# Kernel tuning notes

Measured on AMD Instinct MI355X. Metric: run time of the kernel, lower is better.

## Reference

```python
import jax, jax.numpy as jnp
import numpy as np

N, H, FIN, FOUT = 4096, 8, 128, 64
NEG = -1e9


def setup_inputs() -> dict:
    key = jax.random.key(0)
    ks = jax.random.split(key, 6)
    x = jax.random.normal(ks[0], (N, FIN), dtype=jnp.float32)
    # dense additive adjacency mask: 0 where edge exists, -1e9 otherwise; self-loops on diagonal
    edge = jax.random.uniform(ks[1], (N, N)) < 0.02
    edge = edge | jnp.eye(N, dtype=bool)
    topology = jnp.where(edge, 0.0, NEG).astype(jnp.float32)
    # xavier-ish scaled params
    proj = jax.random.normal(ks[2], (H, FIN, FOUT), dtype=jnp.float32) * (2.0 / (FIN + FOUT)) ** 0.5
    a_src = jax.random.normal(ks[3], (H, FOUT, 1), dtype=jnp.float32) * (2.0 / (FOUT + 1)) ** 0.5
    a_tgt = jax.random.normal(ks[4], (H, FOUT, 1), dtype=jnp.float32) * (2.0 / (FOUT + 1)) ** 0.5
    skip_w = jax.random.normal(ks[5], (H * FOUT, FIN), dtype=jnp.float32) * (1.0 / FIN) ** 0.5
    return {"x": x, "topology": topology, "proj": proj, "a_src": a_src,
            "a_tgt": a_tgt, "skip_w": skip_w}


def reference(x, topology, proj, a_src, a_tgt, skip_w):
    lrelu = lambda v: jax.nn.leaky_relu(v, negative_slope=0.2)
    # projected node features per head: [H, N, FOUT]  (dropout is identity in eval)
    p = jnp.einsum('nf,hfo->hno', x, proj)
    # additive attention scores
    s_src = jnp.einsum('hno,hoi->hn', p, a_src)  # [H, N]
    s_tgt = jnp.einsum('hno,hoi->hn', p, a_tgt)  # [H, N]
    e = lrelu(s_src[:, :, None] + s_tgt[:, None, :])  # [H, N, N]
    attn = jax.nn.softmax(e + topology[None], axis=-1)  # masked row softmax
    # weighted aggregation -> [N, H, FOUT]
    out = jnp.einsum('hnm,hmo->nho', attn, p)
    # skip connection: Fin != Fout so project input
    out = out + (x @ skip_w.T).reshape(N, H, FOUT)
    # heads are averaged (to_aggregate_heads=False), then LeakyReLU
    out = lrelu(jnp.mean(out, axis=1))  # [N, FOUT]
    return out
```

## Files before the change

### kernel.cpp

```cpp
#include <hip/hip_runtime.h>
#include <hip/hip_bf16.h>
#include <cstdint>

#define N_NODES 4096
#define FIN     128
#define FOUT    64
#define NHEAD   8
#define C_TOT   512
#define ECAP    192
#define LDK     136

typedef float fx4    __attribute__((ext_vector_type(4)));
typedef short bf16x8 __attribute__((ext_vector_type(8)));
typedef float f32x4  __attribute__((ext_vector_type(4)));

__device__ __forceinline__ float lrelu(float v){ return v > 0.f ? v : 0.2f*v; }

__device__ __forceinline__ ushort f2b(float f){
    uint u = __float_as_uint(f);
    return (ushort)((u + 0x7FFFu + ((u >> 16) & 1u)) >> 16);
}

__global__ __launch_bounds__(256) void k_gemm(const float* __restrict__ x,
        const float* __restrict__ proj, const float* __restrict__ skip_w,
        const float* __restrict__ a_src, const float* __restrict__ a_tgt,
        __hip_bfloat16* __restrict__ pb, float* __restrict__ s_src_t,
        float* __restrict__ s_tgt_t, float* __restrict__ skipbar){
    __shared__ ushort xs[64*LDK];
    __shared__ ushort bs[64*LDK];
    int tid = threadIdx.x;
    int n0  = blockIdx.x * 64;
    int h   = blockIdx.y;

    #pragma unroll
    for (int k=0; k<8; k++){
        int q = tid + k*256;
        int r = q >> 5, f0 = (q & 31)*4;
        float4 v = *(const float4*)(x + (size_t)(n0+r)*FIN + f0);
        ushort4 u = make_ushort4(f2b(v.x), f2b(v.y), f2b(v.z), f2b(v.w));
        *(ushort4*)(xs + r*LDK + f0) = u;
    }
    if (h < 8){
        const float* B = proj + (size_t)h*FIN*FOUT;
        #pragma unroll
        for (int k=0; k<8; k++){
            int q = tid + k*256;
            int f = q >> 4, o0 = (q & 15)*4;
            float4 v = *(const float4*)(B + f*64 + o0);
            bs[(o0+0)*LDK + f] = f2b(v.x);
            bs[(o0+1)*LDK + f] = f2b(v.y);
            bs[(o0+2)*LDK + f] = f2b(v.z);
            bs[(o0+3)*LDK + f] = f2b(v.w);
        }
    } else {
        #pragma unroll
        for (int k=0; k<8; k++){
            int q = tid + k*256;
            int o = q >> 5, f0 = (q & 31)*4;
            float sx=0.f, sy=0.f, sz=0.f, sw=0.f;
            #pragma unroll
            for (int hh=0; hh<8; hh++){
                float4 v = *(const float4*)(skip_w + (size_t)(hh*64+o)*FIN + f0);
                sx += v.x; sy += v.y; sz += v.z; sw += v.w;
            }
            ushort4 u = make_ushort4(f2b(sx*0.125f), f2b(sy*0.125f),
                                     f2b(sz*0.125f), f2b(sw*0.125f));
            *(ushort4*)(bs + o*LDK + f0) = u;
        }
    }
    __syncthreads();

    int lane = tid & 63, w = tid >> 6;
    int r16 = lane & 15, kg = lane >> 4;
    f32x4 acc[4] = {{0.f,0.f,0.f,0.f},{0.f,0.f,0.f,0.f},
                    {0.f,0.f,0.f,0.f},{0.f,0.f,0.f,0.f}};
    const ushort* arow = xs + (w*16 + r16)*LDK + kg*8;
    #pragma unroll
    for (int ks=0; ks<4; ks++){
        bf16x8 a = *(const bf16x8*)(arow + ks*32);
        #pragma unroll
        for (int ct=0; ct<4; ct++){
            bf16x8 b = *(const bf16x8*)(bs + (ct*16 + r16)*LDK + ks*32 + kg*8);
            acc[ct] = __builtin_amdgcn_mfma_f32_16x16x32_bf16(a, b, acc[ct], 0, 0, 0);
        }
    }

    int rowbase = n0 + w*16 + kg*4;
    if (h < 8){
        float as[4], at[4];
        #pragma unroll
        for (int ct=0; ct<4; ct++){
            as[ct] = a_src[h*64 + ct*16 + r16];
            at[ct] = a_tgt[h*64 + ct*16 + r16];
        }
        ushort* pbu = (ushort*)pb;
        #pragma unroll
        for (int r=0; r<4; r++){
            float vs = 0.f, vt = 0.f;
            #pragma unroll
            for (int ct=0; ct<4; ct++){
                float v = acc[ct][r];
                vs = fmaf(v, as[ct], vs);
                vt = fmaf(v, at[ct], vt);
                pbu[(size_t)(rowbase+r)*C_TOT + (ct*16 + r16)*8 + h] = f2b(v);
            }
            #pragma unroll
            for (int off=1; off<16; off<<=1){
                vs += __shfl_xor(vs, off);
                vt += __shfl_xor(vt, off);
            }
            if (r16 == 0){
                s_src_t[(size_t)(rowbase+r)*8 + h] = vs;
                s_tgt_t[(size_t)(rowbase+r)*8 + h] = vt;
            }
        }
    } else {
        #pragma unroll
        for (int r=0; r<4; r++)
            #pragma unroll
            for (int ct=0; ct<4; ct++)
                skipbar[(size_t)(rowbase+r)*FOUT + ct*16 + r16] = acc[ct][r];
    }
}

__global__ __launch_bounds__(256) void k_fused(const float* __restrict__ topo,
        const __hip_bfloat16* __restrict__ pb, const float* __restrict__ s_src_t,
        const float* __restrict__ s_tgt_t, const float* __restrict__ skipbar,
        float* __restrict__ out){
    __shared__ float  wlds[4*ECAP*8];
    __shared__ ushort jlds[4*ECAP];

    int lane = threadIdx.x & 63, w = threadIdx.x >> 6;
    int i    = blockIdx.x*4 + w;
    float*  wp = wlds + w*(ECAP*8);
    ushort* jp = jlds + w*ECAP;

    jp[lane] = 0; jp[64+lane] = 0; jp[128+lane] = 0;

    const fx4* tp = (const fx4*)(topo + (size_t)i*N_NODES);
    unsigned long long m = 0;
    #pragma unroll
    for (int k=0; k<16; k++){
        fx4 v = __builtin_nontemporal_load(&tp[k*64 + lane]);
        unsigned b = 0;
        b |= (v.x==0.f) ? 1u : 0u;
        b |= (v.y==0.f) ? 2u : 0u;
        b |= (v.z==0.f) ? 4u : 0u;
        b |= (v.w==0.f) ? 8u : 0u;
        m |= ((unsigned long long)b) << (k*4);
    }

    int cnt = __popcll(m);
    int pre = cnt;
    #pragma unroll
    for (int off=1; off<64; off<<=1){
        int t = __shfl_up(pre, off);
        if (lane >= off) pre += t;
    }
    int ne = __shfl(pre, 63);
    if (ne > ECAP) ne = ECAP;
    {
        int base = pre - cnt;
        unsigned long long mm = m;
        while (mm){
            int b = __builtin_ctzll(mm);
            mm &= mm - 1;
            if (base < ECAP)
                jp[base] = (ushort)((b>>2)*256 + lane*4 + (b&3));
            base++;
        }
    }

    float4 ss0 = *(const float4*)(s_src_t + (size_t)i*8);
    float4 ss1 = *(const float4*)(s_src_t + (size_t)i*8 + 4);
    float ssrc[8] = {ss0.x,ss0.y,ss0.z,ss0.w,ss1.x,ss1.y,ss1.z,ss1.w};

    float st[3][8];
    #pragma unroll
    for (int s=0; s<3; s++){
        int e = s*64 + lane;
        bool act = e < ne;
        int j = act ? (int)jp[e] : 0;
        const float4* tpp = (const float4*)(s_tgt_t + (size_t)j*8);
        float4 a = tpp[0], b = tpp[1];
        st[s][0] = act ? a.x : -3.0e38f;
        st[s][1] = act ? a.y : -3.0e38f;
        st[s][2] = act ? a.z : -3.0e38f;
        st[s][3] = act ? a.w : -3.0e38f;
        st[s][4] = act ? b.x : -3.0e38f;
        st[s][5] = act ? b.y : -3.0e38f;
        st[s][6] = act ? b.z : -3.0e38f;
        st[s][7] = act ? b.w : -3.0e38f;
    }
    float M[8];
    #pragma unroll
    for (int hh=0; hh<8; hh++)
        M[hh] = fmaxf(fmaxf(st[0][hh], st[1][hh]), st[2][hh]);
    #pragma unroll
    for (int off=32; off; off>>=1)
        #pragma unroll
        for (int hh=0; hh<8; hh++)
            M[hh] = fmaxf(M[hh], __shfl_xor(M[hh], off));
    #pragma unroll
    for (int hh=0; hh<8; hh++)
        M[hh] = lrelu(ssrc[hh] + M[hh]);

    float den[8] = {0.f,0.f,0.f,0.f,0.f,0.f,0.f,0.f};
    #pragma unroll
    for (int s=0; s<3; s++){
        int e = s*64 + lane;
        bool act = e < ne;
        float wv[8];
        #pragma unroll
        for (int hh=0; hh<8; hh++){
            float z = ssrc[hh] + st[s][hh];
            z = z > 0.f ? z : 0.2f*z;
            float ww = __expf(z - M[hh]);
            ww = act ? ww : 0.f;
            den[hh] += ww;
            wv[hh] = ww;
        }
        *(float4*)(wp + e*8)     = make_float4(wv[0],wv[1],wv[2],wv[3]);
        *(float4*)(wp + e*8 + 4) = make_float4(wv[4],wv[5],wv[6],wv[7]);
    }
    #pragma unroll
    for (int off=32; off; off>>=1)
        #pragma unroll
        for (int hh=0; hh<8; hh++)
            den[hh] += __shfl_xor(den[hh], off);

    float acc[8] = {0.f,0.f,0.f,0.f,0.f,0.f,0.f,0.f};
    const char* pbb = (const char*)pb;
    uint laneoff = (uint)lane * 16;
    int ne8 = (ne + 7) & ~7;
    for (int e0=0; e0<ne8; e0+=8){
        int jj[8];
        #pragma unroll
        for (int k=0; k<8; k++) jj[k] = (int)jp[e0+k];
        uint4 d[8];
        #pragma unroll
        for (int k=0; k<8; k++)
            d[k] = *(const uint4*)(pbb + ((size_t)(uint)jj[k] << 10) + laneoff);
        #pragma unroll
        for (int k=0; k<8; k++){
            float4 wa = *(const float4*)(wp + (e0+k)*8);
            float4 wb = *(const float4*)(wp + (e0+k)*8 + 4);
            acc[0] = fmaf(wa.x, __uint_as_float(d[k].x << 16), acc[0]);
            acc[1] = fmaf(wa.y, __uint_as_float(d[k].x),       acc[1]);
            acc[2] = fmaf(wa.z, __uint_as_float(d[k].y << 16), acc[2]);
            acc[3] = fmaf(wa.w, __uint_as_float(d[k].y),       acc[3]);
            acc[4] = fmaf(wb.x, __uint_as_float(d[k].z << 16), acc[4]);
            acc[5] = fmaf(wb.y, __uint_as_float(d[k].z),       acc[5]);
            acc[6] = fmaf(wb.z, __uint_as_float(d[k].w << 16), acc[6]);
            acc[7] = fmaf(wb.w, __uint_as_float(d[k].w),       acc[7]);
        }
    }

    float s = 0.f;
    #pragma unroll
    for (int hh=0; hh<8; hh++) s += acc[hh] / den[hh];
    float o = s*0.125f + skipbar[(size_t)i*64 + lane];
    out[(size_t)i*64 + lane] = lrelu(o);
}

extern "C" void kernel_launch(void* const* d_in, const int* in_sizes, int n_in,
                              void* d_out, int out_size, void* d_ws, size_t ws_size,
                              hipStream_t stream){
    const float* x      = (const float*)d_in[0];
    const float* topo   = (const float*)d_in[1];
    const float* proj   = (const float*)d_in[2];
    const float* a_src  = (const float*)d_in[3];
    const float* a_tgt  = (const float*)d_in[4];
    const float* skip_w = (const float*)d_in[5];
    float* out = (float*)d_out;

    char* ws = (char*)d_ws;
    __hip_bfloat16* pb = (__hip_bfloat16*)ws;
    float*  skipbar = (float*)(ws + (4u<<20));
    float*  s_src_t = (float*)(ws + (5u<<20));
    float*  s_tgt_t = (float*)(ws + (5u<<20) + (128u<<10));

    hipLaunchKernelGGL(k_gemm,  dim3(64, 9), dim3(256), 0, stream, x, proj, skip_w,
                       a_src, a_tgt, pb, s_src_t, s_tgt_t, skipbar);
    hipLaunchKernelGGL(k_fused, dim3(1024),  dim3(256), 0, stream, topo, pb,
                       s_src_t, s_tgt_t, skipbar, out);
}
```

Before: 47.99 us.

## Split fused kernel into producer wave scanning topology and consumer waves aggregating

Each block now handles 8 nodes. One wave streams the topology rows and builds the neighbour index lists in shared memory, signalling readiness with workgroup-scope release/acquire flags. The other three waves compute the softmax and the aggregation, overlapping the mask scan with the gather/FMA work. Attention weights are stored in shared memory as bf16 to cut LDS footprint, and the index lists are read as vectors. The risk is that a single producer wave per block limits how much of the dominant topology stream is in flight, adds spin-wait overhead, and slightly lowers weight precision.

```diff
diff --git a/kernel.cpp b/kernel.cpp
--- a/kernel.cpp
+++ b/kernel.cpp
@@ -9,6 +9,7 @@
 #define C_TOT   512
 #define ECAP    192
 #define LDK     136
+#define GPB     8
 
 typedef float fx4    __attribute__((ext_vector_type(4)));
 typedef short bf16x8 __attribute__((ext_vector_type(8)));
@@ -127,140 +128,167 @@
         const __hip_bfloat16* __restrict__ pb, const float* __restrict__ s_src_t,
         const float* __restrict__ s_tgt_t, const float* __restrict__ skipbar,
         float* __restrict__ out){
-    __shared__ float  wlds[4*ECAP*8];
-    __shared__ ushort jlds[4*ECAP];
-
-    int lane = threadIdx.x & 63, w = threadIdx.x >> 6;
-    int i    = blockIdx.x*4 + w;
-    float*  wp = wlds + w*(ECAP*8);
-    ushort* jp = jlds + w*ECAP;
-
-    jp[lane] = 0; jp[64+lane] = 0; jp[128+lane] = 0;
-
-    const fx4* tp = (const fx4*)(topo + (size_t)i*N_NODES);
-    unsigned long long m = 0;
-    #pragma unroll
-    for (int k=0; k<16; k++){
-        fx4 v = __builtin_nontemporal_load(&tp[k*64 + lane]);
-        unsigned b = 0;
-        b |= (v.x==0.f) ? 1u : 0u;
-        b |= (v.y==0.f) ? 2u : 0u;
-        b |= (v.z==0.f) ? 4u : 0u;
-        b |= (v.w==0.f) ? 8u : 0u;
-        m |= ((unsigned long long)b) << (k*4);
-    }
-
-    int cnt = __popcll(m);
-    int pre = cnt;
-    #pragma unroll
-    for (int off=1; off<64; off<<=1){
-        int t = __shfl_up(pre, off);
-        if (lane >= off) pre += t;
-    }
-    int ne = __shfl(pre, 63);
-    if (ne > ECAP) ne = ECAP;
-    {
-        int base = pre - cnt;
-        unsigned long long mm = m;
-        while (mm){
-            int b = __builtin_ctzll(mm);
-            mm &= mm - 1;
-            if (base < ECAP)
-                jp[base] = (ushort)((b>>2)*256 + lane*4 + (b&3));
-            base++;
-        }
-    }
-
-    float4 ss0 = *(const float4*)(s_src_t + (size_t)i*8);
-    float4 ss1 = *(const float4*)(s_src_t + (size_t)i*8 + 4);
-    float ssrc[8] = {ss0.x,ss0.y,ss0.z,ss0.w,ss1.x,ss1.y,ss1.z,ss1.w};
-
-    float st[3][8];
-    #pragma unroll
-    for (int s=0; s<3; s++){
-        int e = s*64 + lane;
-        bool act = e < ne;
-        int j = act ? (int)jp[e] : 0;
-        const float4* tpp = (const float4*)(s_tgt_t + (size_t)j*8);
-        float4 a = tpp[0], b = tpp[1];
-        st[s][0] = act ? a.x : -3.0e38f;
-        st[s][1] = act ? a.y : -3.0e38f;
-        st[s][2] = act ? a.z : -3.0e38f;
-        st[s][3] = act ? a.w : -3.0e38f;
-        st[s][4] = act ? b.x : -3.0e38f;
-        st[s][5] = act ? b.y : -3.0e38f;
-        st[s][6] = act ? b.z : -3.0e38f;
-        st[s][7] = act ? b.w : -3.0e38f;
-    }
-    float M[8];
-    #pragma unroll
-    for (int hh=0; hh<8; hh++)
-        M[hh] = fmaxf(fmaxf(st[0][hh], st[1][hh]), st[2][hh]);
-    #pragma unroll
-    for (int off=32; off; off>>=1)
+    __shared__ ushort jlds[GPB*ECAP];
+    __shared__ ushort wbf [3*ECAP*NHEAD];
+    __shared__ int    nelds[GPB];
+    __shared__ int    flagv[GPB];
+
+    int tid  = threadIdx.x;
+    int lane = tid & 63, wv = tid >> 6;
+    int n0   = blockIdx.x * GPB;
+
+    if (tid < GPB) flagv[tid] = 0;
+    __syncthreads();
+
+    if (wv == 3){
+        for (int g=0; g<GPB; g++){
+            int i = n0 + g;
+            const fx4* tp = (const fx4*)(topo + (size_t)i*N_NODES);
+            unsigned long long m = 0;
+            #pragma unroll
+            for (int k=0; k<16; k++){
+                fx4 v = tp[k*64 + lane];
+                unsigned b = 0;
+                b |= (v.x==0.f) ? 1u : 0u;
+                b |= (v.y==0.f) ? 2u : 0u;
+                b |= (v.z==0.f) ? 4u : 0u;
+                b |= (v.w==0.f) ? 8u : 0u;
+                m |= ((unsigned long long)b) << (k*4);
+            }
+            ushort* jp = jlds + g*ECAP;
+            jp[lane] = 0; jp[64+lane] = 0; jp[128+lane] = 0;
+            int cnt = __popcll(m);
+            int pre = cnt;
+            #pragma unroll
+            for (int off=1; off<64; off<<=1){
+                int t = __shfl_up(pre, off);
+                if (lane >= off) pre += t;
+            }
+            int ne = __shfl(pre, 63);
+            if (ne > ECAP) ne = ECAP;
+            int base = pre - cnt;
+            unsigned long long mm = m;
+            while (mm){
+                int b = __builtin_ctzll(mm);
+                mm &= mm - 1;
+                if (base < ECAP)
+                    jp[base] = (ushort)((b>>2)*256 + lane*4 + (b&3));
+                base++;
+            }
+            if (lane == 0) nelds[g] = ne;
+            __hip_atomic_store(&flagv[g], 1, __ATOMIC_RELEASE,
+                               __HIP_MEMORY_SCOPE_WORKGROUP);
+        }
+        return;
+    }
+
+    for (int g = wv; g < GPB; g += 3){
+        int i = n0 + g;
+        int guard = 0;
+        while (__hip_atomic_load(&flagv[g], __ATOMIC_ACQUIRE,
+                                 __HIP_MEMORY_SCOPE_WORKGROUP) == 0){
+            __builtin_amdgcn_s_sleep(2);
+            if (++guard > (1<<24)) break;
+        }
+        int ne = nelds[g];
+        const ushort* jp  = jlds + g*ECAP;
+        ushort*       wpu = wbf  + wv*(ECAP*NHEAD);
+
+        float4 ss0 = *(const float4*)(s_src_t + (size_t)i*8);
+        float4 ss1 = *(const float4*)(s_src_t + (size_t)i*8 + 4);
+        float ssrc[8] = {ss0.x,ss0.y,ss0.z,ss0.w,ss1.x,ss1.y,ss1.z,ss1.w};
+
+        float st[3][8];
+        #pragma unroll
+        for (int s=0; s<3; s++){
+            int e = s*64 + lane;
+            bool act = e < ne;
+            int j = (int)jp[e];
+            const float4* tpp = (const float4*)(s_tgt_t + (size_t)j*8);
+            float4 a = tpp[0], b = tpp[1];
+            st[s][0] = act ? a.x : -3.0e38f;
+            st[s][1] = act ? a.y : -3.0e38f;
+            st[s][2] = act ? a.z : -3.0e38f;
+            st[s][3] = act ? a.w : -3.0e38f;
+            st[s][4] = act ? b.x : -3.0e38f;
+            st[s][5] = act ? b.y : -3.0e38f;
+            st[s][6] = act ? b.z : -3.0e38f;
+            st[s][7] = act ? b.w : -3.0e38f;
+        }
+        float M[8];
         #pragma unroll
         for (int hh=0; hh<8; hh++)
-            M[hh] = fmaxf(M[hh], __shfl_xor(M[hh], off));
-    #pragma unroll
-    for (int hh=0; hh<8; hh++)
-        M[hh] = lrelu(ssrc[hh] + M[hh]);
-
-    float den[8] = {0.f,0.f,0.f,0.f,0.f,0.f,0.f,0.f};
-    #pragma unroll
-    for (int s=0; s<3; s++){
-        int e = s*64 + lane;
-        bool act = e < ne;
-        float wv[8];
-        #pragma unroll
-        for (int hh=0; hh<8; hh++){
-            float z = ssrc[hh] + st[s][hh];
-            z = z > 0.f ? z : 0.2f*z;
-            float ww = __expf(z - M[hh]);
-            ww = act ? ww : 0.f;
-            den[hh] += ww;
-            wv[hh] = ww;
-        }
-        *(float4*)(wp + e*8)     = make_float4(wv[0],wv[1],wv[2],wv[3]);
-        *(float4*)(wp + e*8 + 4) = make_float4(wv[4],wv[5],wv[6],wv[7]);
-    }
-    #pragma unroll
-    for (int off=32; off; off>>=1)
+            M[hh] = fmaxf(fmaxf(st[0][hh], st[1][hh]), st[2][hh]);
+        #pragma unroll
+        for (int off=32; off; off>>=1)
+            #pragma unroll
+            for (int hh=0; hh<8; hh++)
+                M[hh] = fmaxf(M[hh], __shfl_xor(M[hh], off));
         #pragma unroll
         for (int hh=0; hh<8; hh++)
-            den[hh] += __shfl_xor(den[hh], off);
-
-    float acc[8] = {0.f,0.f,0.f,0.f,0.f,0.f,0.f,0.f};
-    const char* pbb = (const char*)pb;
-    uint laneoff = (uint)lane * 16;
-    int ne8 = (ne + 7) & ~7;
-    for (int e0=0; e0<ne8; e0+=8){
-        int jj[8];
-        #pragma unroll
-        for (int k=0; k<8; k++) jj[k] = (int)jp[e0+k];
-        uint4 d[8];
-        #pragma unroll
-        for (int k=0; k<8; k++)
-            d[k] = *(const uint4*)(pbb + ((size_t)(uint)jj[k] << 10) + laneoff);
-        #pragma unroll
-        for (int k=0; k<8; k++){
-            float4 wa = *(const float4*)(wp + (e0+k)*8);
-            float4 wb = *(const float4*)(wp + (e0+k)*8 + 4);
-            acc[0] = fmaf(wa.x, __uint_as_float(d[k].x << 16), acc[0]);
-            acc[1] = fmaf(wa.y, __uint_as_float(d[k].x),       acc[1]);
-            acc[2] = fmaf(wa.z, __uint_as_float(d[k].y << 16), acc[2]);
-            acc[3] = fmaf(wa.w, __uint_as_float(d[k].y),       acc[3]);
-            acc[4] = fmaf(wb.x, __uint_as_float(d[k].z << 16), acc[4]);
-            acc[5] = fmaf(wb.y, __uint_as_float(d[k].z),       acc[5]);
-            acc[6] = fmaf(wb.z, __uint_as_float(d[k].w << 16), acc[6]);
-            acc[7] = fmaf(wb.w, __uint_as_float(d[k].w),       acc[7]);
-        }
-    }
-
-    float s = 0.f;
-    #pragma unroll
-    for (int hh=0; hh<8; hh++) s += acc[hh] / den[hh];
-    float o = s*0.125f + skipbar[(size_t)i*64 + lane];
-    out[(size_t)i*64 + lane] = lrelu(o);
+            M[hh] = lrelu(ssrc[hh] + M[hh]);
+
+        float den[8] = {0.f,0.f,0.f,0.f,0.f,0.f,0.f,0.f};
+        #pragma unroll
+        for (int s=0; s<3; s++){
+            int e = s*64 + lane;
+            bool act = e < ne;
+            float wvv[8];
+            #pragma unroll
+            for (int hh=0; hh<8; hh++){
+                float z = ssrc[hh] + st[s][hh];
+                z = z > 0.f ? z : 0.2f*z;
+                float ww = __expf(z - M[hh]);
+                ww = act ? ww : 0.f;
+                den[hh] += ww;
+                wvv[hh] = ww;
+            }
+            uint p0 = (uint)f2b(wvv[0]) | ((uint)f2b(wvv[1])<<16);
+            uint p1 = (uint)f2b(wvv[2]) | ((uint)f2b(wvv[3])<<16);
+            uint p2 = (uint)f2b(wvv[4]) | ((uint)f2b(wvv[5])<<16);
+            uint p3 = (uint)f2b(wvv[6]) | ((uint)f2b(wvv[7])<<16);
+            *(uint4*)(wpu + e*8) = make_uint4(p0, p1, p2, p3);
+        }
+        #pragma unroll
+        for (int off=32; off; off>>=1)
+            #pragma unroll
+            for (int hh=0; hh<8; hh++)
+                den[hh] += __shfl_xor(den[hh], off);
+
+        float acc[8] = {0.f,0.f,0.f,0.f,0.f,0.f,0.f,0.f};
+        const char* pbb = (const char*)pb;
+        uint laneoff = (uint)lane * 16;
+        int ne8 = (ne + 7) & ~7;
+        for (int e0=0; e0<ne8; e0+=8){
+            uint4 jq = *(const uint4*)(jp + e0);
+            int jj[8] = { (int)(jq.x & 0xffffu), (int)(jq.x >> 16),
+                          (int)(jq.y & 0xffffu), (int)(jq.y >> 16),
+                          (int)(jq.z & 0xffffu), (int)(jq.z >> 16),
+                          (int)(jq.w & 0xffffu), (int)(jq.w >> 16) };
+            uint4 d[8];
+            #pragma unroll
+            for (int k=0; k<8; k++)
+                d[k] = *(const uint4*)(pbb + ((size_t)(uint)jj[k] << 10) + laneoff);
+            #pragma unroll
+            for (int k=0; k<8; k++){
+                uint4 wd = *(const uint4*)(wpu + (e0+k)*8);
+                acc[0] = fmaf(__uint_as_float(wd.x << 16), __uint_as_float(d[k].x << 16), acc[0]);
+                acc[1] = fmaf(__uint_as_float(wd.x),       __uint_as_float(d[k].x),       acc[1]);
+                acc[2] = fmaf(__uint_as_float(wd.y << 16), __uint_as_float(d[k].y << 16), acc[2]);
+                acc[3] = fmaf(__uint_as_float(wd.y),       __uint_as_float(d[k].y),       acc[3]);
+                acc[4] = fmaf(__uint_as_float(wd.z << 16), __uint_as_float(d[k].z << 16), acc[4]);
+                acc[5] = fmaf(__uint_as_float(wd.z),       __uint_as_float(d[k].z),       acc[5]);
+                acc[6] = fmaf(__uint_as_float(wd.w << 16), __uint_as_float(d[k].w << 16), acc[6]);
+                acc[7] = fmaf(__uint_as_float(wd.w),       __uint_as_float(d[k].w),       acc[7]);
+            }
+        }
+
+        float s = 0.f;
+        #pragma unroll
+        for (int hh=0; hh<8; hh++) s += acc[hh] / den[hh];
+        float o = s*0.125f + skipbar[(size_t)i*64 + lane];
+        out[(size_t)i*64 + lane] = lrelu(o);
+    }
 }
 
 extern "C" void kernel_launch(void* const* d_in, const int* in_sizes, int n_in,
@@ -282,6 +310,6 @@
 
     hipLaunchKernelGGL(k_gemm,  dim3(64, 9), dim3(256), 0, stream, x, proj, skip_w,
                        a_src, a_tgt, pb, s_src_t, s_tgt_t, skipbar);
-    hipLaunchKernelGGL(k_fused, dim3(1024),  dim3(256), 0, stream, topo, pb,
+    hipLaunchKernelGGL(k_fused, dim3(N_NODES/GPB), dim3(256), 0, stream, topo, pb,
                        s_src_t, s_tgt_t, skipbar, out);
 }
```

New measurement: 58.43 us. +21.7%, slower.
